# Kernel optimization log

Measured on AMD Instinct MI355X. Metric: run time of the kernel, lower is better.

The kernel has to match this reference:

```python
import math
import jax, jax.numpy as jnp
import numpy as np

# config (matches env defaults of the torch module, scaled to production size)
V, D, L, NH, NKV, MLP_M, RECUR, N_VB = 32768, 1024, 6, 16, 8, 3, 2, 5
BG_BK, BG_DIM = 4096, 128
HD = D // NH            # 64 head dim
KV = NKV * HD           # 512 kv width
B, T = 2, 1024
SOFTCAP = 30.0
EPS = 1.1920929e-07     # fp32 eps used by F.rms_norm(eps=None)


def _rms(x):
    return x * jax.lax.rsqrt(jnp.mean(jnp.square(x), axis=-1, keepdims=True) + EPS)


def _rope(x, c, s):
    h = x.shape[-1] // 2
    x1, x2 = x[..., :h], x[..., h:]
    return jnp.concatenate([x1 * c + x2 * s, -x1 * s + x2 * c], axis=-1)


def _forward(ids, tgt, emb, bg_embed, bg_proj, bg_scale, ve,
             Wq, Wk, Wv, Wo, qg, a_s, m_s, mix, Wfc, Wpr):
    Bz, Tz = ids.shape
    # token embedding + bigram-hash embedding
    x = emb[ids]
    t = ids.astype(jnp.int32)
    hv = jnp.bitwise_xor(t[:, 1:] * 36313, t[:, :-1] * 27191) % (BG_BK - 1)
    h = jnp.zeros_like(t).at[:, 1:].set(hv)
    bg = (bg_embed[h] @ bg_proj) * bg_scale
    x = _rms(x + bg)
    x0 = x
    # rope tables
    inv = 1.0 / (10000.0 ** (jnp.arange(0, HD, 2, dtype=jnp.float32) / HD))
    ang = jnp.arange(Tz, dtype=jnp.float32)[:, None] * inv      # (T, HD/2)
    c, s = jnp.cos(ang)[None, None], jnp.sin(ang)[None, None]   # (1,1,T,HD/2)
    mask = jnp.tril(jnp.ones((Tz, Tz), dtype=bool))
    eff = 0
    for _ in range(RECUR):
        for l in range(L):
            vel = ve[eff % N_VB][ids]                            # (B,T,KV)
            m = mix[l]
            x = m[0] * x + m[1] * x0
            # attention
            xn = _rms(x)
            q = (xn @ Wq[l]).reshape(Bz, Tz, NH, HD).transpose(0, 2, 1, 3)
            k = (xn @ Wk[l]).reshape(Bz, Tz, NKV, HD).transpose(0, 2, 1, 3)
            v = ((xn @ Wv[l]) + vel).reshape(Bz, Tz, NKV, HD).transpose(0, 2, 1, 3)
            q, k = _rms(q), _rms(k)
            q, k = _rope(q, c, s), _rope(k, c, s)
            q = q * qg[l][None, :, None, None]
            rep = NH // NKV                                      # GQA expand
            kf = jnp.repeat(k, rep, axis=1)
            vf = jnp.repeat(v, rep, axis=1)
            sc = jnp.einsum('bhqd,bhkd->bhqk', q, kf) / math.sqrt(HD)
            sc = jnp.where(mask, sc, -jnp.inf)
            att = jax.nn.softmax(sc, axis=-1)
            y = jnp.einsum('bhqk,bhkd->bhqd', att, vf)
            y = y.transpose(0, 2, 1, 3).reshape(Bz, Tz, D) @ Wo[l]
            x = x + a_s[l] * y
            # mlp: relu(fc(x))^2 @ proj
            hmid = jnp.square(jax.nn.relu(_rms(x) @ Wfc[l]))
            x = x + m_s[l] * (hmid @ Wpr[l])
            eff += 1
    x = _rms(x)
    lo = x @ emb.T
    lo = SOFTCAP * jnp.tanh(lo / SOFTCAP)
    logp = jax.nn.log_softmax(lo, axis=-1)
    nll = -jnp.take_along_axis(logp, tgt[..., None], axis=-1)[..., 0]
    return jnp.mean(nll)


def setup_inputs() -> dict:
    key = jax.random.key(0)
    ks = jax.random.split(key, 14)
    def nrm(k, shape, std):
        return std * jax.random.normal(k, shape, dtype=jnp.float32)
    eff = L * RECUR
    return {
        'ids': jax.random.randint(ks[0], (B, T), 0, V),
        'tgt': jax.random.randint(ks[1], (B, T), 0, V),
        'emb': nrm(ks[2], (V, D), 0.005),
        'bg_embed': nrm(ks[3], (BG_BK, BG_DIM), 0.02),
        'bg_proj': nrm(ks[4], (BG_DIM, D), 1.0 / math.sqrt(BG_DIM)),
        'bg_scale': jnp.float32(0.05),
        've': nrm(ks[5], (N_VB, V, KV), 0.01),
        'Wq': nrm(ks[6], (L, D, D), 1.0 / math.sqrt(D)),
        'Wk': nrm(ks[7], (L, D, KV), 1.0 / math.sqrt(D)),
        'Wv': nrm(ks[8], (L, D, KV), 1.0 / math.sqrt(D)),
        'Wo': nrm(ks[9], (L, D, D), 1.0 / (math.sqrt(D) * math.sqrt(2 * eff))),
        'qg': jnp.full((L, NH), 1.5, jnp.float32),
        'a_s': jnp.ones((L, D), jnp.float32),
        'm_s': jnp.ones((L, D), jnp.float32),
        'mix': jnp.stack([jnp.ones((L, D)), jnp.zeros((L, D))], axis=1).astype(jnp.float32),
        'Wfc': nrm(ks[10], (L, D, MLP_M * D), 1.0 / math.sqrt(D)),
        'Wpr': nrm(ks[11], (L, MLP_M * D, D), 1.0 / (math.sqrt(MLP_M * D) * math.sqrt(2 * eff))),
    }


def reference(ids, tgt, emb, bg_embed, bg_proj, bg_scale, ve,
              Wq, Wk, Wv, Wo, qg, a_s, m_s, mix, Wfc, Wpr):
    return _forward(ids, tgt, emb, bg_embed, bg_proj, bg_scale, ve,
                    Wq, Wk, Wv, Wo, qg, a_s, m_s, mix, Wfc, Wpr)
```

## Files before the change

### kernel.cpp

```cpp
#include <hip/hip_runtime.h>
#include <hip/hip_bf16.h>
#include <math.h>

#define DEV __device__ __forceinline__

typedef unsigned short u16;
typedef short bf16x8 __attribute__((ext_vector_type(8)));
typedef float f32x4 __attribute__((ext_vector_type(4)));
typedef u16 u16x8 __attribute__((ext_vector_type(8)));
typedef u16 u16x4 __attribute__((ext_vector_type(4)));

#define T_SEQ 1024
#define NTOK 2048
#define DIM 1024
#define NHD 16
#define NKVH 8
#define HDIM 64
#define KVD 512
#define MLPD 3072
#define VOC 32768
#define EPSF 1.1920929e-07f
#define SCAP 30.0f
#define NCB 512
#define PSTRIDE ((size_t)NTOK * DIM)

#define MEMFENCE asm volatile("" ::: "memory")

DEV u16 f2b(float f) {
  __hip_bfloat16 h = __float2bfloat16(f);
  u16 r; __builtin_memcpy(&r, &h, 2); return r;
}
DEV float b2f(u16 u) {
  __hip_bfloat16 h; __builtin_memcpy(&h, &u, 2);
  return __bfloat162float(h);
}

DEV void gload16(const void* g, void* l) {
  __builtin_amdgcn_global_load_lds((const __attribute__((address_space(1))) void*)g,
                                   (__attribute__((address_space(3))) void*)l, 16, 0, 0);
}

DEV float blk_sum256(float v, float* sbuf) {
#pragma unroll
  for (int o = 32; o; o >>= 1) v += __shfl_xor(v, o, 64);
  int w = threadIdx.x >> 6;
  if ((threadIdx.x & 63) == 0) sbuf[w] = v;
  __syncthreads();
  return sbuf[0] + sbuf[1] + sbuf[2] + sbuf[3];
}

__global__ __launch_bounds__(256) void prep_all(
    const float* __restrict__ Wq, const float* __restrict__ Wk, const float* __restrict__ Wv,
    const float* __restrict__ Wo, const float* __restrict__ Wfc, const float* __restrict__ Wpr,
    const float* __restrict__ emb,
    u16* __restrict__ WqkvT, u16* __restrict__ WoT, u16* __restrict__ WfcT,
    u16* __restrict__ WprT, u16* __restrict__ embB,
    float* __restrict__ rc, float* __restrict__ rs,
    const int* __restrict__ ids, const float* __restrict__ bg_embed,
    const float* __restrict__ bg_proj, const float* __restrict__ bg_scale_p,
    const float* __restrict__ mix0,
    float* __restrict__ x, float* __restrict__ x0, u16* __restrict__ xn) {
  int bid = blockIdx.x;
  int tid = threadIdx.x;
  if (bid < 55296) {
    const float* in; u16* out; int nx, K, N; size_t in_ls, out_ls; int base;
    if (bid < 6144)       { base = 0;     in = Wq;  out = WqkvT;           nx = 32; K = 1024; N = 1024; in_ls = 1048576; out_ls = 2097152; }
    else if (bid < 9216)  { base = 6144;  in = Wk;  out = WqkvT + 1048576; nx = 16; K = 1024; N = 512;  in_ls = 524288;  out_ls = 2097152; }
    else if (bid < 12288) { base = 9216;  in = Wv;  out = WqkvT + 1572864; nx = 16; K = 1024; N = 512;  in_ls = 524288;  out_ls = 2097152; }
    else if (bid < 18432) { base = 12288; in = Wo;  out = WoT;             nx = 32; K = 1024; N = 1024; in_ls = 1048576; out_ls = 1048576; }
    else if (bid < 36864) { base = 18432; in = Wfc; out = WfcT;            nx = 96; K = 1024; N = 3072; in_ls = 3145728; out_ls = 3145728; }
    else                  { base = 36864; in = Wpr; out = WprT;            nx = 32; K = 3072; N = 1024; in_ls = 3145728; out_ls = 3145728; }
    int local = bid - base;
    int kx = local % nx;
    int rest = local / nx;
    int ny = K >> 5;
    int ky = rest % ny;
    int l = rest / ny;
    __shared__ float tile[32][33];
    const float* src = in + (size_t)l * in_ls;
    u16* dst = out + (size_t)l * out_ls;
    int k0 = ky << 5, n0 = kx << 5;
    int tx = tid & 31, ty = tid >> 5;
#pragma unroll
    for (int i = 0; i < 32; i += 8)
      tile[ty + i][tx] = src[(size_t)(k0 + ty + i) * N + n0 + tx];
    __syncthreads();
#pragma unroll
    for (int i = 0; i < 32; i += 8)
      dst[(size_t)(n0 + ty + i) * K + k0 + tx] = f2b(tile[tx][ty + i]);
  } else if (bid < 71680) {
    size_t i = ((size_t)(bid - 55296) * 256 + tid) * 8;
    float4 a = *(const float4*)(emb + i);
    float4 b = *(const float4*)(emb + i + 4);
    u16x8 o;
    o[0] = f2b(a.x); o[1] = f2b(a.y); o[2] = f2b(a.z); o[3] = f2b(a.w);
    o[4] = f2b(b.x); o[5] = f2b(b.y); o[6] = f2b(b.z); o[7] = f2b(b.w);
    *(u16x8*)(embB + i) = o;
  } else if (bid < 71808) {
    int idx = (bid - 71680) * 256 + tid;
    int t = idx >> 5, i2 = idx & 31;
    float inv = expf(-((float)(2 * i2) / (float)HDIM) * logf(10000.0f));
    float ang = (float)t * inv;
    rc[idx] = cosf(ang);
    rs[idx] = sinf(ang);
  } else {
    __shared__ float be[128];
    __shared__ float sbuf[4];
    int tok = bid - 71808;
    int t = tok & (T_SEQ - 1);
    int id = ids[tok];
    int hsh = 0;
    if (t > 0) {
      int prev = ids[tok - 1];
      hsh = ((id * 36313) ^ (prev * 27191)) % 4095;
    }
    if (tid < 128) be[tid] = bg_embed[hsh * 128 + tid];
    __syncthreads();
    float scale = bg_scale_p[0];
    const float4* bp = (const float4*)bg_proj;
    float ax = 0.f, ay = 0.f, az = 0.f, aw = 0.f;
#pragma unroll 4
    for (int j = 0; j < 128; ++j) {
      float bj = be[j];
      float4 p = bp[j * 256 + tid];
      ax += bj * p.x; ay += bj * p.y; az += bj * p.z; aw += bj * p.w;
    }
    float4 e = *(const float4*)(emb + (size_t)id * DIM + tid * 4);
    float vx = e.x + ax * scale, vy = e.y + ay * scale;
    float vz = e.z + az * scale, vw = e.w + aw * scale;
    float ss = vx * vx + vy * vy + vz * vz + vw * vw;
    float tot = blk_sum256(ss, sbuf);
    float rn = rsqrtf(tot * (1.0f / DIM) + EPSF);
    float4 o; o.x = vx * rn; o.y = vy * rn; o.z = vz * rn; o.w = vw * rn;
    size_t base = (size_t)tok * DIM + tid * 4;
    *(float4*)(x0 + base) = o;
    float4 m0 = *(const float4*)(mix0 + tid * 4);
    float4 m1 = *(const float4*)(mix0 + DIM + tid * 4);
    float4 a;
    a.x = (m0.x + m1.x) * o.x;
    a.y = (m0.y + m1.y) * o.y;
    a.z = (m0.z + m1.z) * o.z;
    a.w = (m0.w + m1.w) * o.w;
    *(float4*)(x + base) = a;
    __syncthreads();
    float ss2 = a.x * a.x + a.y * a.y + a.z * a.z + a.w * a.w;
    float tot2 = blk_sum256(ss2, sbuf);
    float rn2 = rsqrtf(tot2 * (1.0f / DIM) + EPSF);
    u16x4 q;
    q[0] = f2b(a.x * rn2); q[1] = f2b(a.y * rn2); q[2] = f2b(a.z * rn2); q[3] = f2b(a.w * rn2);
    *(u16x4*)(xn + base) = q;
  }
}

template <int NP, int MIX>
__global__ __launch_bounds__(256) void norm_k(float* __restrict__ x,
    const u16* __restrict__ parts, const float* __restrict__ colscale,
    const float* __restrict__ mixl, const float* __restrict__ x0,
    u16* __restrict__ xn) {
  __shared__ float sbuf[4];
  int tok = blockIdx.x, tid = threadIdx.x;
  size_t base = (size_t)tok * DIM + tid * 4;
  float4 a = *(const float4*)(x + base);
  if (NP > 0) {
    float4 cs = *(const float4*)(colscale + tid * 4);
    u16x4 p0 = *(const u16x4*)(parts + base);
    u16x4 p1 = *(const u16x4*)(parts + PSTRIDE + base);
    float sx = b2f(p0[0]) + b2f(p1[0]);
    float sy = b2f(p0[1]) + b2f(p1[1]);
    float sz = b2f(p0[2]) + b2f(p1[2]);
    float sw = b2f(p0[3]) + b2f(p1[3]);
    if (NP == 3) {
      u16x4 p2 = *(const u16x4*)(parts + 2 * PSTRIDE + base);
      sx += b2f(p2[0]); sy += b2f(p2[1]); sz += b2f(p2[2]); sw += b2f(p2[3]);
    }
    a.x += cs.x * sx; a.y += cs.y * sy; a.z += cs.z * sz; a.w += cs.w * sw;
  }
  if (MIX) {
    float4 m0 = *(const float4*)(mixl + tid * 4);
    float4 m1 = *(const float4*)(mixl + DIM + tid * 4);
    float4 b = *(const float4*)(x0 + base);
    a.x = m0.x * a.x + m1.x * b.x;
    a.y = m0.y * a.y + m1.y * b.y;
    a.z = m0.z * a.z + m1.z * b.z;
    a.w = m0.w * a.w + m1.w * b.w;
  }
  float ss = a.x * a.x + a.y * a.y + a.z * a.z + a.w * a.w;
  float tot = blk_sum256(ss, sbuf);
  float rn = rsqrtf(tot * (1.0f / DIM) + EPSF);
  if (NP > 0 || MIX) *(float4*)(x + base) = a;
  u16x4 q;
  q[0] = f2b(a.x * rn); q[1] = f2b(a.y * rn); q[2] = f2b(a.z * rn); q[3] = f2b(a.w * rn);
  *(u16x4*)(xn + base) = q;
}

template <int EPI, int BN>
__global__ __launch_bounds__(256, (BN == 64 ? 3 : 2)) void gemm_bt(
    const u16* __restrict__ A, const u16* __restrict__ Bt,
    u16* __restrict__ Cb,
    int N, int K, int kpn) {
  constexpr int MF = (BN == 128) ? 4 : 2;
  constexpr int ASZ = 128 * 64;
  constexpr int BSZ = BN * 64;
  constexpr int NLD = 4 + BN / 32;
  __shared__ u16 As[2 * ASZ];
  __shared__ u16 Bs[2 * BSZ];
  int tid = threadIdx.x;
  int wid = tid >> 6, lane = tid & 63;
  int g = lane >> 4, c = lane & 15;
  int row0 = blockIdx.y << 7, col0 = blockIdx.x * BN;
  int kbase = blockIdx.z * kpn;
  int wr = (BN == 128) ? ((wid >> 1) << 6) : (wid << 5);
  int wc = (BN == 128) ? ((wid & 1) << 6) : 0;
  f32x4 acc[MF][4] = {};

  int sr = lane >> 3;
  int kb = lane & 7;
  const u16* srcA[4];
  int ldsA[4];
#pragma unroll
  for (int i = 0; i < 4; ++i) {
    int s = (wid << 2) + i;
    int r = (s << 3) + sr;
    srcA[i] = A + (size_t)(row0 + r) * K + kbase + ((kb ^ (r & 7)) << 3);
    ldsA[i] = s << 9;
  }
  const u16* srcB[BN / 32];
  int ldsB[BN / 32];
#pragma unroll
  for (int i = 0; i < BN / 32; ++i) {
    int s = wid * (BN / 32) + i;
    int r = (s << 3) + sr;
    srcB[i] = Bt + (size_t)(col0 + r) * K + kbase + ((kb ^ (r & 7)) << 3);
    ldsB[i] = s << 9;
  }

#pragma unroll
  for (int i = 0; i < 4; ++i) gload16(srcA[i], As + ldsA[i]);
#pragma unroll
  for (int i = 0; i < BN / 32; ++i) gload16(srcB[i], Bs + ldsB[i]);

  int nk = kpn >> 6;
  for (int t = 0; t < nk; ++t) {
    int cur = t & 1;
    if (t + 1 < nk) {
      int nxt = cur ^ 1;
      int ko = (t + 1) << 6;
#pragma unroll
      for (int i = 0; i < 4; ++i) gload16(srcA[i] + ko, As + nxt * ASZ + ldsA[i]);
#pragma unroll
      for (int i = 0; i < BN / 32; ++i) gload16(srcB[i] + ko, Bs + nxt * BSZ + ldsB[i]);
      if constexpr (NLD == 6) asm volatile("s_waitcnt vmcnt(6)" ::: "memory");
      else asm volatile("s_waitcnt vmcnt(8)" ::: "memory");
    } else {
      asm volatile("s_waitcnt vmcnt(0)" ::: "memory");
    }
    __builtin_amdgcn_s_barrier();
    MEMFENCE;
    const u16* ab = As + cur * ASZ;
    const u16* bb = Bs + cur * BSZ;
#pragma unroll
    for (int ks = 0; ks < 2; ++ks) {
      bf16x8 af[MF], bfr[4];
#pragma unroll
      for (int m = 0; m < MF; ++m) {
        int r = wr + m * 16 + c;
        int kbs = ((ks << 2) + g) ^ (r & 7);
        af[m] = *(const bf16x8*)(ab + r * 64 + (kbs << 3));
      }
#pragma unroll
      for (int n = 0; n < 4; ++n) {
        int r = wc + n * 16 + c;
        int kbs = ((ks << 2) + g) ^ (r & 7);
        bfr[n] = *(const bf16x8*)(bb + r * 64 + (kbs << 3));
      }
      __builtin_amdgcn_s_setprio(1);
#pragma unroll
      for (int m = 0; m < MF; ++m)
#pragma unroll
        for (int n = 0; n < 4; ++n)
          acc[m][n] = __builtin_amdgcn_mfma_f32_16x16x32_bf16(af[m], bfr[n], acc[m][n], 0, 0, 0);
      __builtin_amdgcn_s_setprio(0);
    }
    MEMFENCE;
    __builtin_amdgcn_s_barrier();
  }

  size_t zoff = (size_t)blockIdx.z * PSTRIDE;
#pragma unroll
  for (int m = 0; m < MF; ++m) {
#pragma unroll
    for (int n = 0; n < 4; ++n) {
      int gcol = col0 + wc + n * 16 + c;
#pragma unroll
      for (int j = 0; j < 4; ++j) {
        int grow = row0 + wr + m * 16 + g * 4 + j;
        float v = acc[m][n][j];
        if (EPI == 1) {
          Cb[zoff + (size_t)grow * N + gcol] = f2b(v);
        } else if (EPI == 2) {
          float r = v > 0.f ? v : 0.f;
          Cb[(size_t)grow * N + gcol] = f2b(r * r);
        }
      }
    }
  }
}

__global__ __launch_bounds__(512, 2) void gemm_lmhead(
    const u16* __restrict__ A, const u16* __restrict__ Bt,
    const int* __restrict__ tgt, float* __restrict__ pM, float* __restrict__ pS,
    float* __restrict__ loTgt) {
  constexpr int K = 1024;
  constexpr int TSZ = 256 * 64;
  __shared__ u16 As[2 * TSZ];
  __shared__ u16 Bs[2 * TSZ];
  int tid = threadIdx.x;
  int wid = tid >> 6, lane = tid & 63;
  int wm = wid >> 2, wn = wid & 3;
  int g = lane >> 4, c = lane & 15;
  int bid = blockIdx.x;
  int swz = ((bid & 7) << 7) + (bid >> 3);
  int colb = swz >> 3, rowb = swz & 7;
  int row0 = rowb << 8, col0 = colb << 8;
  f32x4 acc[8][4] = {};

  int sr = lane >> 3, kb = lane & 7;
  const u16* srcA[4];
  const u16* srcB[4];
  int ldsOff[4];
#pragma unroll
  for (int i = 0; i < 4; ++i) {
    int s = (wid << 2) + i;
    int r = (s << 3) + sr;
    srcA[i] = A + (size_t)(row0 + r) * K + ((kb ^ (r & 7)) << 3);
    srcB[i] = Bt + (size_t)(col0 + r) * K + ((kb ^ (r & 7)) << 3);
    ldsOff[i] = s << 9;
  }

#pragma unroll
  for (int i = 0; i < 4; ++i) {
    gload16(srcA[i], As + ldsOff[i]);
    gload16(srcB[i], Bs + ldsOff[i]);
  }

  constexpr int nk = K >> 6;
  for (int kt = 0; kt < nk; ++kt) {
    int cur = kt & 1;
    if (kt + 1 < nk) {
      int nxt = cur ^ 1;
      int ko = (kt + 1) << 6;
#pragma unroll
      for (int i = 0; i < 4; ++i) {
        gload16(srcA[i] + ko, As + nxt * TSZ + ldsOff[i]);
        gload16(srcB[i] + ko, Bs + nxt * TSZ + ldsOff[i]);
      }
      asm volatile("s_waitcnt vmcnt(8)" ::: "memory");
    } else {
      asm volatile("s_waitcnt vmcnt(0)" ::: "memory");
    }
    __builtin_amdgcn_s_barrier();
    MEMFENCE;
    const u16* ab = As + cur * TSZ;
    const u16* bb = Bs + cur * TSZ;
    bf16x8 bfr[4][2];
#pragma unroll
    for (int nf = 0; nf < 4; ++nf) {
      int r = (wn << 6) + nf * 16 + c;
#pragma unroll
      for (int ks = 0; ks < 2; ++ks) {
        int kbs = ((ks << 2) + g) ^ (r & 7);
        bfr[nf][ks] = *(const bf16x8*)(bb + r * 64 + (kbs << 3));
      }
    }
#pragma unroll
    for (int p = 0; p < 4; ++p) {
      bf16x8 af[2][2];
#pragma unroll
      for (int mi = 0; mi < 2; ++mi) {
        int r = (wm << 7) + ((p << 1) + mi) * 16 + c;
#pragma unroll
        for (int ks = 0; ks < 2; ++ks) {
          int kbs = ((ks << 2) + g) ^ (r & 7);
          af[mi][ks] = *(const bf16x8*)(ab + r * 64 + (kbs << 3));
        }
      }
      __builtin_amdgcn_s_setprio(1);
#pragma unroll
      for (int ks = 0; ks < 2; ++ks)
#pragma unroll
        for (int mi = 0; mi < 2; ++mi)
#pragma unroll
          for (int nf = 0; nf < 4; ++nf)
            acc[(p << 1) + mi][nf] = __builtin_amdgcn_mfma_f32_16x16x32_bf16(
                af[mi][ks], bfr[nf][ks], acc[(p << 1) + mi][nf], 0, 0, 0);
      __builtin_amdgcn_s_setprio(0);
    }
    MEMFENCE;
    __builtin_amdgcn_s_barrier();
  }

  int cb = (col0 >> 6) + wn;
#pragma unroll
  for (int mf = 0; mf < 8; ++mf) {
#pragma unroll
    for (int j = 0; j < 4; ++j) {
      int grow = row0 + (wm << 7) + mf * 16 + g * 4 + j;
      int tg = tgt[grow];
      float sv[4];
      float mx = -3.0e38f;
#pragma unroll
      for (int nf = 0; nf < 4; ++nf) {
        float a = acc[mf][nf][j] * (1.0f / SCAP);
        a = fminf(fmaxf(a, -15.f), 15.f);
        float e = __expf(2.0f * a);
        float tt = SCAP * (e - 1.0f) / (e + 1.0f);
        sv[nf] = tt;
        mx = fmaxf(mx, tt);
        int gcol = col0 + (wn << 6) + nf * 16 + c;
        if (gcol == tg) loTgt[grow] = tt;
      }
      mx = fmaxf(mx, __shfl_xor(mx, 1, 64));
      mx = fmaxf(mx, __shfl_xor(mx, 2, 64));
      mx = fmaxf(mx, __shfl_xor(mx, 4, 64));
      mx = fmaxf(mx, __shfl_xor(mx, 8, 64));
      float s = 0.f;
#pragma unroll
      for (int nf = 0; nf < 4; ++nf) s += __expf(sv[nf] - mx);
      s += __shfl_xor(s, 1, 64);
      s += __shfl_xor(s, 2, 64);
      s += __shfl_xor(s, 4, 64);
      s += __shfl_xor(s, 8, 64);
      if (c == 0) {
        pM[(size_t)grow * NCB + cb] = mx;
        pS[(size_t)grow * NCB + cb] = s;
      }
    }
  }
}

__global__ __launch_bounds__(256, 3) void gemm_qkv(
    const u16* __restrict__ A, const u16* __restrict__ Bt,
    const float* __restrict__ qg_l, const float* __restrict__ rc, const float* __restrict__ rs,
    const float* __restrict__ ve, const int* __restrict__ ids, int vb,
    u16* __restrict__ qB, u16* __restrict__ kB, u16* __restrict__ vT) {
  constexpr int K = 1024;
  constexpr int ASZ = 128 * 64;
  constexpr int BSZ = 64 * 64;
  __shared__ u16 As[2 * ASZ];
  __shared__ u16 Bs[2 * BSZ];
  int tid = threadIdx.x;
  int wid = tid >> 6, lane = tid & 63;
  int g = lane >> 4, c = lane & 15;
  int bx = blockIdx.x;
  int row0 = blockIdx.y << 7, col0 = bx << 6;
  f32x4 acc[2][4] = {};

  int sr = lane >> 3, kb = lane & 7;
  const u16* srcA[4];
  int ldsA[4];
#pragma unroll
  for (int i = 0; i < 4; ++i) {
    int s = (wid << 2) + i;
    int r = (s << 3) + sr;
    srcA[i] = A + (size_t)(row0 + r) * K + ((kb ^ (r & 7)) << 3);
    ldsA[i] = s << 9;
  }
  const u16* srcB[2];
  int ldsB[2];
#pragma unroll
  for (int i = 0; i < 2; ++i) {
    int s = (wid << 1) + i;
    int r = (s << 3) + sr;
    srcB[i] = Bt + (size_t)(col0 + r) * K + ((kb ^ (r & 7)) << 3);
    ldsB[i] = s << 9;
  }

#pragma unroll
  for (int i = 0; i < 4; ++i) gload16(srcA[i], As + ldsA[i]);
#pragma unroll
  for (int i = 0; i < 2; ++i) gload16(srcB[i], Bs + ldsB[i]);

  for (int t = 0; t < 16; ++t) {
    int cur = t & 1;
    if (t + 1 < 16) {
      int nxt = cur ^ 1;
      int ko = (t + 1) << 6;
#pragma unroll
      for (int i = 0; i < 4; ++i) gload16(srcA[i] + ko, As + nxt * ASZ + ldsA[i]);
#pragma unroll
      for (int i = 0; i < 2; ++i) gload16(srcB[i] + ko, Bs + nxt * BSZ + ldsB[i]);
      asm volatile("s_waitcnt vmcnt(6)" ::: "memory");
    } else {
      asm volatile("s_waitcnt vmcnt(0)" ::: "memory");
    }
    __builtin_amdgcn_s_barrier();
    MEMFENCE;
    const u16* ab = As + cur * ASZ;
    const u16* bb = Bs + cur * BSZ;
#pragma unroll
    for (int ks = 0; ks < 2; ++ks) {
      bf16x8 af[2], bfr[4];
#pragma unroll
      for (int m = 0; m < 2; ++m) {
        int r = (wid << 5) + m * 16 + c;
        int kbs = ((ks << 2) + g) ^ (r & 7);
        af[m] = *(const bf16x8*)(ab + r * 64 + (kbs << 3));
      }
#pragma unroll
      for (int n = 0; n < 4; ++n) {
        int r = n * 16 + c;
        int kbs = ((ks << 2) + g) ^ (r & 7);
        bfr[n] = *(const bf16x8*)(bb + r * 64 + (kbs << 3));
      }
      __builtin_amdgcn_s_setprio(1);
#pragma unroll
      for (int m = 0; m < 2; ++m)
#pragma unroll
        for (int n = 0; n < 4; ++n)
          acc[m][n] = __builtin_amdgcn_mfma_f32_16x16x32_bf16(af[m], bfr[n], acc[m][n], 0, 0, 0);
      __builtin_amdgcn_s_setprio(0);
    }
    MEMFENCE;
    __builtin_amdgcn_s_barrier();
  }

  int b = row0 >> 10;
  if (bx < 24) {
    bool isq = (bx < 16);
    int h = isq ? bx : bx - 16;
    float gmul = isq ? qg_l[h] * 0.125f : 1.0f;
    u16* hb = isq ? (qB + ((size_t)(b * NHD + h)) * T_SEQ * HDIM)
                  : (kB + ((size_t)(b * NKVH + h)) * T_SEQ * HDIM);
#pragma unroll
    for (int m = 0; m < 2; ++m) {
#pragma unroll
      for (int j = 0; j < 4; ++j) {
        int grow = row0 + (wid << 5) + m * 16 + g * 4 + j;
        int t = grow & (T_SEQ - 1);
        float vv[4];
        float ss = 0.f;
#pragma unroll
        for (int n = 0; n < 4; ++n) { vv[n] = acc[m][n][j]; ss += vv[n] * vv[n]; }
        ss += __shfl_xor(ss, 1, 64);
        ss += __shfl_xor(ss, 2, 64);
        ss += __shfl_xor(ss, 4, 64);
        ss += __shfl_xor(ss, 8, 64);
        float rn = rsqrtf(ss * (1.0f / HDIM) + EPSF);
#pragma unroll
        for (int n = 0; n < 4; ++n) vv[n] *= rn;
        float c0 = rc[t * 32 + c], s0 = rs[t * 32 + c];
        float c1 = rc[t * 32 + 16 + c], s1 = rs[t * 32 + 16 + c];
        float o0 = vv[0] * c0 + vv[2] * s0;
        float o1 = vv[1] * c1 + vv[3] * s1;
        float o2 = vv[2] * c0 - vv[0] * s0;
        float o3 = vv[3] * c1 - vv[1] * s1;
        u16* dst = hb + (size_t)t * HDIM;
        dst[c] = f2b(o0 * gmul);
        dst[16 + c] = f2b(o1 * gmul);
        dst[32 + c] = f2b(o2 * gmul);
        dst[48 + c] = f2b(o3 * gmul);
      }
    }
  } else {
    int kh = bx - 24;
#pragma unroll
    for (int m = 0; m < 2; ++m) {
#pragma unroll
      for (int j = 0; j < 4; ++j) {
        int grow = row0 + (wid << 5) + m * 16 + g * 4 + j;
        int lr = (wid << 5) + m * 16 + g * 4 + j;
        int id = ids[grow];
        const float* vl = ve + ((size_t)vb * VOC + id) * KVD + kh * HDIM;
#pragma unroll
        for (int n = 0; n < 4; ++n)
          As[lr * 72 + n * 16 + c] = f2b(acc[m][n][j] + vl[n * 16 + c]);
      }
    }
    __syncthreads();
    int hd = tid & 63, seg = tid >> 6;
    int t0 = (row0 & (T_SEQ - 1)) + seg * 32;
    u16* dst = vT + (((size_t)(b * NKVH + kh)) * HDIM + hd) * T_SEQ + t0;
#pragma unroll
    for (int i = 0; i < 32; i += 8) {
      u16x8 o;
#pragma unroll
      for (int e = 0; e < 8; ++e) o[e] = As[(seg * 32 + i + e) * 72 + hd];
      *(u16x8*)(dst + i) = o;
    }
  }
}

__global__ __launch_bounds__(128) void attn_kernel(const u16* __restrict__ qB,
    const u16* __restrict__ kB, const u16* __restrict__ vT, const float* __restrict__ qg_l,
    u16* __restrict__ attout) {
  __shared__ u16 plds[2][32 * 76];
  int b = blockIdx.z, h = blockIdx.y;
  int kh = h >> 1;
  int wid = threadIdx.x >> 6, lane = threadIdx.x & 63;
  int g = lane >> 4, c = lane & 15;
  int strip = wid ? (31 - (int)blockIdx.x) : (int)blockIdx.x;
  int qr0 = strip << 5;
  const u16* qptr = qB + ((size_t)(b * NHD + h)) * T_SEQ * HDIM;
  const u16* kptr = kB + ((size_t)(b * NKVH + kh)) * T_SEQ * HDIM;
  const u16* vptr = vT + ((size_t)(b * NKVH + kh)) * HDIM * T_SEQ;
  u16* pw = plds[wid];
  float Mh = fabsf(qg_l[h]) * 8.0f;

  bf16x8 aq[2][2];
#pragma unroll
  for (int m = 0; m < 2; ++m)
#pragma unroll
    for (int ks = 0; ks < 2; ++ks)
      aq[m][ks] = *(const bf16x8*)(qptr + (qr0 + m * 16 + c) * HDIM + ks * 32 + g * 8);

  bf16x8 vone;
#pragma unroll
  for (int e = 0; e < 8; ++e) vone[e] = (short)0x3F80;

  f32x4 oacc[2][4] = {};
  f32x4 lacc[2] = {};

  bf16x8 kR0[4][2], vR0[4][2], kR1[4][2], vR1[4][2];

  auto LOADKV = [&](bf16x8 (&bk)[4][2], bf16x8 (&bv)[4][2], int kv0) {
#pragma unroll
    for (int n = 0; n < 4; ++n)
#pragma unroll
      for (int ks = 0; ks < 2; ++ks) {
        bk[n][ks] = *(const bf16x8*)(kptr + (kv0 + n * 16 + c) * HDIM + ks * 32 + g * 8);
        bv[n][ks] = *(const bf16x8*)(vptr + (n * 16 + c) * T_SEQ + kv0 + ks * 32 + g * 8);
      }
  };

  auto BODY = [&](bf16x8 (&bk)[4][2], bf16x8 (&bv)[4][2], int kv0) {
    f32x4 sc[2][4] = {};
#pragma unroll
    for (int ks = 0; ks < 2; ++ks)
#pragma unroll
      for (int m = 0; m < 2; ++m)
#pragma unroll
        for (int n = 0; n < 4; ++n)
          sc[m][n] = __builtin_amdgcn_mfma_f32_16x16x32_bf16(aq[m][ks], bk[n][ks], sc[m][n], 0, 0, 0);
    bool maskT = (kv0 + 64 > qr0);
#pragma unroll
    for (int m = 0; m < 2; ++m) {
#pragma unroll
      for (int j = 0; j < 4; ++j) {
        int row = qr0 + m * 16 + g * 4 + j;
        float p0 = __expf(sc[m][0][j] - Mh);
        float p1 = __expf(sc[m][1][j] - Mh);
        float p2 = __expf(sc[m][2][j] - Mh);
        float p3 = __expf(sc[m][3][j] - Mh);
        if (maskT) {
          if (kv0 + c > row) p0 = 0.f;
          if (kv0 + 16 + c > row) p1 = 0.f;
          if (kv0 + 32 + c > row) p2 = 0.f;
          if (kv0 + 48 + c > row) p3 = 0.f;
        }
        int pr = m * 16 + g * 4 + j;
        pw[pr * 76 + c] = f2b(p0);
        pw[pr * 76 + 16 + c] = f2b(p1);
        pw[pr * 76 + 32 + c] = f2b(p2);
        pw[pr * 76 + 48 + c] = f2b(p3);
      }
    }
    MEMFENCE;
    bf16x8 ap[2][2];
#pragma unroll
    for (int m = 0; m < 2; ++m)
#pragma unroll
      for (int ks = 0; ks < 2; ++ks) {
        u16x8 tmp = *(const u16x8*)(pw + (m * 16 + c) * 76 + ks * 32 + g * 8);
        __builtin_memcpy(&ap[m][ks], &tmp, 16);
      }
#pragma unroll
    for (int ks = 0; ks < 2; ++ks) {
#pragma unroll
      for (int m = 0; m < 2; ++m) {
#pragma unroll
        for (int n = 0; n < 4; ++n)
          oacc[m][n] = __builtin_amdgcn_mfma_f32_16x16x32_bf16(ap[m][ks], bv[n][ks], oacc[m][n], 0, 0, 0);
        lacc[m] = __builtin_amdgcn_mfma_f32_16x16x32_bf16(ap[m][ks], vone, lacc[m], 0, 0, 0);
      }
    }
  };

  LOADKV(kR0, vR0, 0);
  int kv0 = 0;
  while (true) {
    if (kv0 + 64 <= qr0) LOADKV(kR1, vR1, kv0 + 64);
    BODY(kR0, vR0, kv0);
    kv0 += 64;
    if (kv0 > qr0) break;
    if (kv0 + 64 <= qr0) LOADKV(kR0, vR0, kv0 + 64);
    BODY(kR1, vR1, kv0);
    kv0 += 64;
    if (kv0 > qr0) break;
  }

#pragma unroll
  for (int m = 0; m < 2; ++m) {
#pragma unroll
    for (int j = 0; j < 4; ++j) {
      float inv = 1.0f / lacc[m][j];
      int trow = qr0 + m * 16 + g * 4 + j;
      u16* orow = attout + ((size_t)(b * T_SEQ + trow)) * DIM + h * HDIM;
#pragma unroll
      for (int n = 0; n < 4; ++n)
        orow[n * 16 + c] = f2b(oacc[m][n][j] * inv);
    }
  }
}

__global__ __launch_bounds__(256) void lse_merge(const float* __restrict__ pM,
    const float* __restrict__ pS, const float* __restrict__ loTgt, float* __restrict__ nll) {
  __shared__ float sbuf[4];
  int tok = blockIdx.x, tid = threadIdx.x;
  int wid = tid >> 6, lane = tid & 63;
  const float* rm = pM + (size_t)tok * NCB;
  const float* rs = pS + (size_t)tok * NCB;
  float m0 = rm[tid], m1 = rm[tid + 256];
  float mx = fmaxf(m0, m1);
#pragma unroll
  for (int o = 32; o; o >>= 1) mx = fmaxf(mx, __shfl_xor(mx, o, 64));
  if (lane == 0) sbuf[wid] = mx;
  __syncthreads();
  float M = fmaxf(fmaxf(sbuf[0], sbuf[1]), fmaxf(sbuf[2], sbuf[3]));
  __syncthreads();
  float s = rs[tid] * __expf(m0 - M) + rs[tid + 256] * __expf(m1 - M);
  float S = blk_sum256(s, sbuf);
  if (tid == 0) nll[tok] = logf(S) + M - loTgt[tok];
}

__global__ __launch_bounds__(256) void loss_final(const float* __restrict__ nll,
    float* __restrict__ out) {
  __shared__ float sbuf[4];
  int tid = threadIdx.x;
  float acc = 0.f;
  for (int i = tid; i < NTOK; i += 256) acc += nll[i];
  float tot = blk_sum256(acc, sbuf);
  if (tid == 0) out[0] = tot * (1.0f / NTOK);
}

extern "C" void kernel_launch(void* const* d_in, const int* in_sizes, int n_in,
                              void* d_out, int out_size, void* d_ws, size_t ws_size,
                              hipStream_t stream) {
  (void)in_sizes; (void)n_in; (void)out_size; (void)ws_size;
  const int* ids = (const int*)d_in[0];
  const int* tgt = (const int*)d_in[1];
  const float* emb = (const float*)d_in[2];
  const float* bg_embed = (const float*)d_in[3];
  const float* bg_proj = (const float*)d_in[4];
  const float* bg_scale = (const float*)d_in[5];
  const float* ve = (const float*)d_in[6];
  const float* Wq = (const float*)d_in[7];
  const float* Wk = (const float*)d_in[8];
  const float* Wv = (const float*)d_in[9];
  const float* Wo = (const float*)d_in[10];
  const float* qg = (const float*)d_in[11];
  const float* a_s = (const float*)d_in[12];
  const float* m_s = (const float*)d_in[13];
  const float* mix = (const float*)d_in[14];
  const float* Wfc = (const float*)d_in[15];
  const float* Wpr = (const float*)d_in[16];

  char* w = (char*)d_ws;
  auto alloc = [&](size_t bytes) {
    char* p = w;
    w += (bytes + 255) & ~(size_t)255;
    return p;
  };
  u16* WqkvT = (u16*)alloc(6ull * 2048 * 1024 * 2);
  u16* WoT   = (u16*)alloc(6ull * 1024 * 1024 * 2);
  u16* WfcT  = (u16*)alloc(6ull * 3072 * 1024 * 2);
  u16* WprT  = (u16*)alloc(6ull * 1024 * 3072 * 2);
  u16* embB  = (u16*)alloc((size_t)VOC * DIM * 2);
  float* x   = (float*)alloc((size_t)NTOK * DIM * 4);
  float* x0  = (float*)alloc((size_t)NTOK * DIM * 4);
  u16* xn    = (u16*)alloc((size_t)NTOK * DIM * 2);
  u16* qBuf  = (u16*)alloc((size_t)NTOK * DIM * 2);
  u16* kBuf  = (u16*)alloc((size_t)NTOK * KVD * 2);
  u16* vTb   = (u16*)alloc((size_t)NTOK * KVD * 2);
  u16* attout = (u16*)alloc((size_t)NTOK * DIM * 2);
  u16* xmlp  = (u16*)alloc((size_t)NTOK * DIM * 2);
  u16* hmid  = (u16*)alloc((size_t)NTOK * MLPD * 2);
  u16* pparts = (u16*)alloc(3 * PSTRIDE * 2);
  float* rc  = (float*)alloc((size_t)T_SEQ * 32 * 4);
  float* rs  = (float*)alloc((size_t)T_SEQ * 32 * 4);
  float* pM  = (float*)alloc((size_t)NTOK * NCB * 4);
  float* pS  = (float*)alloc((size_t)NTOK * NCB * 4);
  float* loTgt = (float*)alloc(NTOK * 4);
  float* nll = (float*)alloc(NTOK * 4);

  prep_all<<<73856, 256, 0, stream>>>(Wq, Wk, Wv, Wo, Wfc, Wpr, emb,
      WqkvT, WoT, WfcT, WprT, embB, rc, rs,
      ids, bg_embed, bg_proj, bg_scale, mix, x, x0, xn);

  int lprev = 0;
  for (int step = 0; step < 12; ++step) {
    int l = step % 6;
    if (step > 0)
      norm_k<3, 1><<<NTOK, 256, 0, stream>>>(x, pparts, m_s + lprev * DIM, mix + l * 2048, x0, xn);
    gemm_qkv<<<dim3(32, 16), 256, 0, stream>>>(xn, WqkvT + (size_t)l * 2048 * 1024,
        qg + l * 16, rc, rs, ve, ids, step % 5, qBuf, kBuf, vTb);
    attn_kernel<<<dim3(16, 16, 2), 128, 0, stream>>>(qBuf, kBuf, vTb, qg + l * 16, attout);
    gemm_bt<1, 64><<<dim3(16, 16, 2), 256, 0, stream>>>(attout, WoT + (size_t)l * 1024 * 1024,
        pparts, 1024, 1024, 512);
    norm_k<2, 0><<<NTOK, 256, 0, stream>>>(x, pparts, a_s + l * DIM, nullptr, nullptr, xmlp);
    gemm_bt<2, 64><<<dim3(48, 16, 1), 256, 0, stream>>>(xmlp, WfcT + (size_t)l * 3072 * 1024,
        hmid, 3072, 1024, 1024);
    gemm_bt<1, 64><<<dim3(16, 16, 3), 256, 0, stream>>>(hmid, WprT + (size_t)l * 1024 * 3072,
        pparts, 1024, 3072, 1024);
    lprev = l;
  }

  norm_k<3, 0><<<NTOK, 256, 0, stream>>>(x, pparts, m_s + lprev * DIM, nullptr, nullptr, xn);
  gemm_lmhead<<<1024, 512, 0, stream>>>(xn, embB, tgt, pM, pS, loTgt);
  lse_merge<<<NTOK, 256, 0, stream>>>(pM, pS, loTgt, nll);
  loss_final<<<1, 256, 0, stream>>>(nll, (float*)d_out);
}
```

Measured before the change: 1.770 ms.

## Interleave A/B global-to-LDS staging across MFMA phases in LM-head GEMM

```diff
diff --git a/kernel.cpp b/kernel.cpp
--- a/kernel.cpp
+++ b/kernel.cpp
@@ -325,65 +325,83 @@
   f32x4 acc[8][4] = {};
 
   int sr = lane >> 3, kb = lane & 7;
-  const u16* srcA[4];
-  const u16* srcB[4];
-  int ldsOff[4];
-#pragma unroll
-  for (int i = 0; i < 4; ++i) {
-    int s = (wid << 2) + i;
-    int r = (s << 3) + sr;
-    srcA[i] = A + (size_t)(row0 + r) * K + ((kb ^ (r & 7)) << 3);
-    srcB[i] = Bt + (size_t)(col0 + r) * K + ((kb ^ (r & 7)) << 3);
-    ldsOff[i] = s << 9;
-  }
-
-#pragma unroll
-  for (int i = 0; i < 4; ++i) {
-    gload16(srcA[i], As + ldsOff[i]);
-    gload16(srcB[i], Bs + ldsOff[i]);
-  }
-
-  constexpr int nk = K >> 6;
-  for (int kt = 0; kt < nk; ++kt) {
-    int cur = kt & 1;
-    if (kt + 1 < nk) {
-      int nxt = cur ^ 1;
-      int ko = (kt + 1) << 6;
-#pragma unroll
-      for (int i = 0; i < 4; ++i) {
-        gload16(srcA[i] + ko, As + nxt * TSZ + ldsOff[i]);
-        gload16(srcB[i] + ko, Bs + nxt * TSZ + ldsOff[i]);
-      }
-      asm volatile("s_waitcnt vmcnt(8)" ::: "memory");
-    } else {
-      asm volatile("s_waitcnt vmcnt(0)" ::: "memory");
-    }
-    __builtin_amdgcn_s_barrier();
-    MEMFENCE;
-    const u16* ab = As + cur * TSZ;
-    const u16* bb = Bs + cur * TSZ;
-    bf16x8 bfr[4][2];
-#pragma unroll
-    for (int nf = 0; nf < 4; ++nf) {
-      int r = (wn << 6) + nf * 16 + c;
-#pragma unroll
-      for (int ks = 0; ks < 2; ++ks) {
-        int kbs = ((ks << 2) + g) ^ (r & 7);
-        bfr[nf][ks] = *(const bf16x8*)(bb + r * 64 + (kbs << 3));
-      }
-    }
-#pragma unroll
-    for (int p = 0; p < 4; ++p) {
+  const u16* srcA[2][2];
+  const u16* srcB[2][2];
+  int ldsOff[2][2];
+#pragma unroll
+  for (int h = 0; h < 2; ++h)
+#pragma unroll
+    for (int i = 0; i < 2; ++i) {
+      int s = (h << 4) + (wid << 1) + i;
+      int r = (s << 3) + sr;
+      srcA[h][i] = A + (size_t)(row0 + r) * K + ((kb ^ (r & 7)) << 3);
+      srcB[h][i] = Bt + (size_t)(col0 + r) * K + ((kb ^ (r & 7)) << 3);
+      ldsOff[h][i] = s << 9;
+    }
+
+  auto stageA = [&](int T, int h) {
+    int ko = T << 6;
+    int bo = (T & 1) * TSZ;
+#pragma unroll
+    for (int i = 0; i < 2; ++i) gload16(srcA[h][i] + ko, As + bo + ldsOff[h][i]);
+  };
+  auto stageB = [&](int T, int h) {
+    int ko = T << 6;
+    int bo = (T & 1) * TSZ;
+#pragma unroll
+    for (int i = 0; i < 2; ++i) gload16(srcB[h][i] + ko, Bs + bo + ldsOff[h][i]);
+  };
+
+  stageB(0, 0); stageB(0, 1);
+  stageA(0, 0); stageA(0, 1);
+  stageB(1, 0); stageB(1, 1);
+
+  bf16x8 bfr[4][2];
+  for (int kt2 = 0; kt2 < 16; kt2 += 2) {
+#pragma unroll
+    for (int p = 0; p < 8; ++p) {
+      int tt = p >> 2;
+      int q = p & 3;
+      int bo = tt * TSZ;
+      if (p == 0) {
+        asm volatile("s_waitcnt vmcnt(4)" ::: "memory");
+      } else if (p == 4) {
+        if (kt2 == 14) { asm volatile("s_waitcnt vmcnt(0)" ::: "memory"); }
+        else           { asm volatile("s_waitcnt vmcnt(4)" ::: "memory"); }
+      }
+      __builtin_amdgcn_s_barrier();
+      MEMFENCE;
+      if (q == 0) {
+#pragma unroll
+        for (int nf = 0; nf < 4; ++nf) {
+          int r = (wn << 6) + nf * 16 + c;
+#pragma unroll
+          for (int ks = 0; ks < 2; ++ks) {
+            int kbs = ((ks << 2) + g) ^ (r & 7);
+            bfr[nf][ks] = *(const bf16x8*)(Bs + bo + r * 64 + (kbs << 3));
+          }
+        }
+      }
       bf16x8 af[2][2];
 #pragma unroll
       for (int mi = 0; mi < 2; ++mi) {
-        int r = (wm << 7) + ((p << 1) + mi) * 16 + c;
+        int r = (wm << 7) + ((q << 1) + mi) * 16 + c;
 #pragma unroll
         for (int ks = 0; ks < 2; ++ks) {
           int kbs = ((ks << 2) + g) ^ (r & 7);
-          af[mi][ks] = *(const bf16x8*)(ab + r * 64 + (kbs << 3));
+          af[mi][ks] = *(const bf16x8*)(As + bo + r * 64 + (kbs << 3));
         }
       }
+      if (p == 0)      { stageA(kt2 + 1, 0); }
+      else if (p == 1) { stageA(kt2 + 1, 1); }
+      else if (p == 2) { if (kt2 + 2 < 16) stageB(kt2 + 2, 0); }
+      else if (p == 3) { if (kt2 + 2 < 16) stageB(kt2 + 2, 1); }
+      else if (p == 4) { if (kt2 + 2 < 16) stageA(kt2 + 2, 0); }
+      else if (p == 5) { if (kt2 + 2 < 16) stageA(kt2 + 2, 1); }
+      else if (p == 6) { if (kt2 + 3 < 16) stageB(kt2 + 3, 0); }
+      else             { if (kt2 + 3 < 16) stageB(kt2 + 3, 1); }
+      MEMFENCE;
+      __builtin_amdgcn_s_barrier();
       __builtin_amdgcn_s_setprio(1);
 #pragma unroll
       for (int ks = 0; ks < 2; ++ks)
@@ -391,12 +409,10 @@
         for (int mi = 0; mi < 2; ++mi)
 #pragma unroll
           for (int nf = 0; nf < 4; ++nf)
-            acc[(p << 1) + mi][nf] = __builtin_amdgcn_mfma_f32_16x16x32_bf16(
-                af[mi][ks], bfr[nf][ks], acc[(p << 1) + mi][nf], 0, 0, 0);
+            acc[(q << 1) + mi][nf] = __builtin_amdgcn_mfma_f32_16x16x32_bf16(
+                af[mi][ks], bfr[nf][ks], acc[(q << 1) + mi][nf], 0, 0, 0);
       __builtin_amdgcn_s_setprio(0);
     }
-    MEMFENCE;
-    __builtin_amdgcn_s_barrier();
   }
 
   int cb = (col0 >> 6) + wn;
```

Measured after the change: 1.743 ms, median of 2. No clear change (-1.5%).
